# Kernel optimization log

Hardware: AMD Instinct MI355X
Metric: run time of the kernel (lower is better)

The kernel has to match this reference:

```python
import jax, jax.numpy as jnp
import numpy as np

SCALE_WEIGHT = 0.5 ** 0.5
B, C, T, S = 8, 512, 2048, 2048


def setup_inputs() -> dict:
    key = jax.random.key(0)
    ks = jax.random.split(key, 6)
    return {
        "base_target_emb": jax.random.normal(ks[0], (B, C, T, 1), dtype=jnp.float32),
        "input_from_dec": jax.random.normal(ks[1], (B, C, T, 1), dtype=jnp.float32),
        "encoder_out_top": jax.random.normal(ks[2], (B, C, S), dtype=jnp.float32),
        "encoder_out_combine": jax.random.normal(ks[3], (B, C, S), dtype=jnp.float32),
        "W": jax.random.normal(ks[4], (C, C), dtype=jnp.float32) * (1.0 / np.sqrt(C)),
        "b": jax.random.normal(ks[5], (C,), dtype=jnp.float32) * 0.01,
    }


def reference(base_target_emb, input_from_dec, encoder_out_top, encoder_out_combine, W, b):
    # seq_linear: per-token Linear over the channel dim. torch Linear: h = x @ W.T + b, W is [out,in]
    x = input_from_dec[..., 0]                                # [B,C,T]
    preatt = jnp.einsum('oc,bct->bot', W, x) + b[None, :, None]  # [B,C,T]
    target = (base_target_emb[..., 0] + preatt) * SCALE_WEIGHT   # [B,C,T]
    pre_attn = jnp.einsum('bct,bcs->bts', target, encoder_out_top)  # [B,T,S]
    attn = jax.nn.softmax(pre_attn, axis=2)                      # [B,T,S]
    ctx = jnp.einsum('bts,bcs->btc', attn, encoder_out_combine)  # [B,T,C]
    context_output = jnp.transpose(ctx, (0, 2, 1))[..., None]    # [B,C,T,1]
    return context_output, attn
```

## Files before the change

### kernel.cpp

```cpp
#include <hip/hip_runtime.h>
#include <cstddef>
#include <cstdint>

#define SCALE_WEIGHT 0.70710678118654752440f

static constexpr int B_ = 8, C_ = 512, T_ = 2048, S_ = 2048;
static constexpr size_t BCT_ = (size_t)B_ * C_ * T_;
static constexpr size_t BTS_ = (size_t)B_ * T_ * S_;

typedef _Float16 half_t;
typedef half_t half8  __attribute__((ext_vector_type(8)));
typedef half_t half4v __attribute__((ext_vector_type(4)));
typedef float  floatx4 __attribute__((ext_vector_type(4)));

__device__ __forceinline__ void gload_lds16(const void* g, void* l) {
    __builtin_amdgcn_global_load_lds(
        (const __attribute__((address_space(1))) void*)g,
        (__attribute__((address_space(3))) void*)l, 16, 0, 0);
}

__global__ __launch_bounds__(256) void transpose2_cvt_kernel(
    const float* __restrict__ x, const float* __restrict__ top,
    half_t* __restrict__ xT, half_t* __restrict__ topT)
{
    __shared__ float tile[64][65];
    const int z = blockIdx.z;
    const float* in = (z < 8) ? x : top;
    half_t* outp = (z < 8) ? xT : topT;
    const int b  = z & 7;
    const int r0 = blockIdx.y * 64, c0 = blockIdx.x * 64;
    const float* ib = in + (size_t)b * C_ * T_;
    half_t* ob = outp + (size_t)b * C_ * T_;
    const int t  = threadIdx.x;
    const int rr = t >> 4, cq = t & 15;
    #pragma unroll
    for (int i = 0; i < 4; ++i) {
        const int r = rr + i * 16;
        float4 v = *(const float4*)&ib[(size_t)(r0 + r) * T_ + c0 + cq * 4];
        tile[cq * 4 + 0][r] = v.x;
        tile[cq * 4 + 1][r] = v.y;
        tile[cq * 4 + 2][r] = v.z;
        tile[cq * 4 + 3][r] = v.w;
    }
    __syncthreads();
    const int cw = t >> 4, rq = (t & 15) * 4;
    #pragma unroll
    for (int i = 0; i < 4; ++i) {
        const int c = cw + i * 16;
        half4v h = {(half_t)tile[c][rq + 0], (half_t)tile[c][rq + 1],
                    (half_t)tile[c][rq + 2], (half_t)tile[c][rq + 3]};
        *(half4v*)&ob[(size_t)(c0 + c) * C_ + r0 + rq] = h;
    }
}

__global__ __launch_bounds__(256) void cvt2_f32_f16_kernel(
    const float* __restrict__ comb, half_t* __restrict__ combh,
    const float* __restrict__ W, half_t* __restrict__ Wh,
    int n4a, int n4tot)
{
    const int stride = gridDim.x * blockDim.x;
    for (int i = blockIdx.x * blockDim.x + threadIdx.x; i < n4tot; i += stride) {
        const float4* src; half4v* dst; int j;
        if (i < n4a) { src = (const float4*)comb; dst = (half4v*)combh; j = i; }
        else         { src = (const float4*)W;    dst = (half4v*)Wh;    j = i - n4a; }
        float4 v = src[j];
        dst[j] = (half4v){(half_t)v.x, (half_t)v.y, (half_t)v.z, (half_t)v.w};
    }
}

template<int EPI>
__global__ __launch_bounds__(256) void gemm_f16_db_kernel(
    const half_t* __restrict__ A, const half_t* __restrict__ Bm,
    float* __restrict__ Cout, half_t* __restrict__ CoutH,
    const float* __restrict__ base, const float* __restrict__ bias,
    int M, int N, int K, size_t sA, size_t sB, size_t sC)
{
    __shared__ __align__(128) half_t As[2][128 * 64];
    __shared__ __align__(128) half_t Bs[2][128 * 64];

    const int tid  = threadIdx.x;
    const int lane = tid & 63, w = tid >> 6;
    const int wr = w >> 1, wc = w & 1;
    const int b  = blockIdx.z;
    const int m0 = blockIdx.y * 128, n0 = blockIdx.x * 128;

    const half_t* Ab = A  + (size_t)b * sA;
    const half_t* Bb = Bm + (size_t)b * sB;

    const int lr = lane >> 3;
    const int sw = (lane & 7) ^ lr;
    const half_t* aG[4]; const half_t* bG[4];
    int dOff[4];
    #pragma unroll
    for (int i = 0; i < 4; ++i) {
        const int r = w * 32 + i * 8 + lr;
        aG[i] = Ab + (size_t)(m0 + r) * K + sw * 8;
        bG[i] = Bb + (size_t)(n0 + r) * K + sw * 8;
        dOff[i] = (w * 32 + i * 8) * 128;
    }

    const int fr = lane & 15, kg = lane >> 4;
    int aoff[4], boff[4];
    #pragma unroll
    for (int mi = 0; mi < 4; ++mi) {
        const int m = wr * 64 + mi * 16 + fr;
        aoff[mi] = m * 128 + ((kg ^ (m & 7)) << 4);
    }
    #pragma unroll
    for (int nj = 0; nj < 4; ++nj) {
        const int n = wc * 64 + nj * 16 + fr;
        boff[nj] = n * 128 + ((kg ^ (n & 7)) << 4);
    }

    floatx4 acc[4][4];
    #pragma unroll
    for (int mi = 0; mi < 4; ++mi)
        #pragma unroll
        for (int nj = 0; nj < 4; ++nj)
            acc[mi][nj] = (floatx4){0.f, 0.f, 0.f, 0.f};

    auto STAGE = [&](int t, int pg) {
        const int k0 = t * 64;
        char* Ad = (char*)As[pg];
        char* Bd = (char*)Bs[pg];
        #pragma unroll
        for (int i = 0; i < 4; ++i) {
            gload_lds16(aG[i] + k0, Ad + dOff[i]);
            gload_lds16(bG[i] + k0, Bd + dOff[i]);
        }
    };

    auto COMPUTE = [&](int pg) {
        const char* Ar = (const char*)As[pg];
        const char* Br = (const char*)Bs[pg];
        #pragma unroll
        for (int kk = 0; kk < 2; ++kk) {
            half8 af[4], bf[4];
            #pragma unroll
            for (int mi = 0; mi < 4; ++mi)
                af[mi] = *(const half8*)(Ar + (aoff[mi] ^ (kk << 6)));
            #pragma unroll
            for (int nj = 0; nj < 4; ++nj)
                bf[nj] = *(const half8*)(Br + (boff[nj] ^ (kk << 6)));
            #pragma unroll
            for (int mi = 0; mi < 4; ++mi)
                #pragma unroll
                for (int nj = 0; nj < 4; ++nj)
                    acc[mi][nj] = __builtin_amdgcn_mfma_f32_16x16x32_f16(
                        af[mi], bf[nj], acc[mi][nj], 0, 0, 0);
        }
    };

    const int NT = K >> 6;
    STAGE(0, 0);
    int cur = 0;
    for (int t = 0; t < NT - 1; ++t) {
        STAGE(t + 1, cur ^ 1);
        asm volatile("s_waitcnt vmcnt(8)" ::: "memory");
        __builtin_amdgcn_s_barrier();
        __builtin_amdgcn_sched_barrier(0);
        COMPUTE(cur);
        asm volatile("s_waitcnt lgkmcnt(0)" ::: "memory");
        __builtin_amdgcn_sched_barrier(0);
        __builtin_amdgcn_s_barrier();
        __builtin_amdgcn_sched_barrier(0);
        cur ^= 1;
    }
    asm volatile("s_waitcnt vmcnt(0)" ::: "memory");
    __builtin_amdgcn_s_barrier();
    __builtin_amdgcn_sched_barrier(0);
    COMPUTE(cur);

    if constexpr (EPI == 0) {
        float* Cb = Cout + (size_t)b * sC;
        #pragma unroll
        for (int mi = 0; mi < 4; ++mi) {
            const int row = m0 + wr * 64 + mi * 16 + (lane >> 4) * 4;
            #pragma unroll
            for (int nj = 0; nj < 4; ++nj) {
                const int col = n0 + wc * 64 + nj * 16 + (lane & 15);
                #pragma unroll
                for (int r = 0; r < 4; ++r)
                    Cb[(size_t)(row + r) * N + col] = acc[mi][nj][r];
            }
        }
    } else {
        half_t* Cb = CoutH + (size_t)b * sC;
        #pragma unroll
        for (int nj = 0; nj < 4; ++nj) {
            const int col = n0 + wc * 64 + nj * 16 + (lane & 15);
            const float bn = bias[col];
            const float* bp = base + ((size_t)b * N + col) * (size_t)M;
            #pragma unroll
            for (int mi = 0; mi < 4; ++mi) {
                const int row = m0 + wr * 64 + mi * 16 + (lane >> 4) * 4;
                #pragma unroll
                for (int r = 0; r < 4; ++r) {
                    float v = (acc[mi][nj][r] + bn + bp[row + r]) * SCALE_WEIGHT;
                    Cb[(size_t)(row + r) * N + col] = (half_t)v;
                }
            }
        }
    }
}

__global__ __launch_bounds__(256) void k2p_kernel(
    const half_t* __restrict__ A, const half_t* __restrict__ Bm,
    half_t* __restrict__ P, float* __restrict__ mArr, float* __restrict__ sArr)
{
    __shared__ __align__(128) half_t As[2][128 * 64];
    __shared__ __align__(128) half_t Bs[2][128 * 64];
    __shared__ float rmax[2][128];
    __shared__ float rsum[2][128];

    const int tid  = threadIdx.x;
    const int lane = tid & 63, w = tid >> 6;
    const int wr = w >> 1, wc = w & 1;
    const int b  = blockIdx.z;
    const int m0 = blockIdx.y * 128, n0 = blockIdx.x * 128;
    constexpr int K = C_;

    const half_t* Ab = A  + (size_t)b * T_ * C_;
    const half_t* Bb = Bm + (size_t)b * S_ * C_;

    const int lr = lane >> 3;
    const int sw = (lane & 7) ^ lr;
    const half_t* aG[4]; const half_t* bG[4];
    int dOff[4];
    #pragma unroll
    for (int i = 0; i < 4; ++i) {
        const int r = w * 32 + i * 8 + lr;
        aG[i] = Ab + (size_t)(m0 + r) * K + sw * 8;
        bG[i] = Bb + (size_t)(n0 + r) * K + sw * 8;
        dOff[i] = (w * 32 + i * 8) * 128;
    }

    const int fr = lane & 15, kg = lane >> 4;
    const int q4 = kg * 4;
    int aoff[4], boff[4];
    #pragma unroll
    for (int mi = 0; mi < 4; ++mi) {
        const int m = wr * 64 + mi * 16 + fr;
        aoff[mi] = m * 128 + ((kg ^ (m & 7)) << 4);
    }
    #pragma unroll
    for (int nj = 0; nj < 4; ++nj) {
        const int n = wc * 64 + nj * 16 + fr;
        boff[nj] = n * 128 + ((kg ^ (n & 7)) << 4);
    }

    floatx4 acc[4][4];
    #pragma unroll
    for (int mi = 0; mi < 4; ++mi)
        #pragma unroll
        for (int nj = 0; nj < 4; ++nj)
            acc[mi][nj] = (floatx4){0.f, 0.f, 0.f, 0.f};

    auto STAGE = [&](int t, int pg) {
        const int k0 = t * 64;
        char* Ad = (char*)As[pg];
        char* Bd = (char*)Bs[pg];
        #pragma unroll
        for (int i = 0; i < 4; ++i) {
            gload_lds16(aG[i] + k0, Ad + dOff[i]);
            gload_lds16(bG[i] + k0, Bd + dOff[i]);
        }
    };

    auto COMPUTE = [&](int pg) {
        const char* Ar = (const char*)As[pg];
        const char* Br = (const char*)Bs[pg];
        #pragma unroll
        for (int kk = 0; kk < 2; ++kk) {
            half8 af[4], bf[4];
            #pragma unroll
            for (int mi = 0; mi < 4; ++mi)
                af[mi] = *(const half8*)(Ar + (aoff[mi] ^ (kk << 6)));
            #pragma unroll
            for (int nj = 0; nj < 4; ++nj)
                bf[nj] = *(const half8*)(Br + (boff[nj] ^ (kk << 6)));
            #pragma unroll
            for (int mi = 0; mi < 4; ++mi)
                #pragma unroll
                for (int nj = 0; nj < 4; ++nj)
                    acc[mi][nj] = __builtin_amdgcn_mfma_f32_16x16x32_f16(
                        af[mi], bf[nj], acc[mi][nj], 0, 0, 0);
        }
    };

    constexpr int NT = K >> 6;
    STAGE(0, 0);
    int cur = 0;
    for (int t = 0; t < NT - 1; ++t) {
        STAGE(t + 1, cur ^ 1);
        asm volatile("s_waitcnt vmcnt(8)" ::: "memory");
        __builtin_amdgcn_s_barrier();
        __builtin_amdgcn_sched_barrier(0);
        COMPUTE(cur);
        asm volatile("s_waitcnt lgkmcnt(0)" ::: "memory");
        __builtin_amdgcn_sched_barrier(0);
        __builtin_amdgcn_s_barrier();
        __builtin_amdgcn_sched_barrier(0);
        cur ^= 1;
    }
    asm volatile("s_waitcnt vmcnt(0)" ::: "memory");
    __builtin_amdgcn_s_barrier();
    __builtin_amdgcn_sched_barrier(0);
    COMPUTE(cur);

    #pragma unroll
    for (int mi = 0; mi < 4; ++mi) {
        #pragma unroll
        for (int r = 0; r < 4; ++r) {
            float v = fmaxf(fmaxf(acc[mi][0][r], acc[mi][1][r]),
                            fmaxf(acc[mi][2][r], acc[mi][3][r]));
            v = fmaxf(v, __shfl_xor(v, 1));
            v = fmaxf(v, __shfl_xor(v, 2));
            v = fmaxf(v, __shfl_xor(v, 4));
            v = fmaxf(v, __shfl_xor(v, 8));
            if (fr == 0) rmax[wc][wr * 64 + mi * 16 + q4 + r] = v;
        }
    }
    __syncthreads();

    half_t* Pb = P + ((size_t)(b * T_ + m0)) * S_;
    #pragma unroll
    for (int mi = 0; mi < 4; ++mi) {
        #pragma unroll
        for (int r = 0; r < 4; ++r) {
            const int row = wr * 64 + mi * 16 + q4 + r;
            const float mC = fmaxf(rmax[0][row], rmax[1][row]);
            float s = 0.f;
            #pragma unroll
            for (int nj = 0; nj < 4; ++nj) {
                float pv = __expf(acc[mi][nj][r] - mC);
                s += pv;
                Pb[(size_t)row * S_ + n0 + wc * 64 + nj * 16 + fr] = (half_t)pv;
            }
            s += __shfl_xor(s, 1);
            s += __shfl_xor(s, 2);
            s += __shfl_xor(s, 4);
            s += __shfl_xor(s, 8);
            if (fr == 0) rsum[wc][row] = s;
        }
    }
    __syncthreads();

    if (tid < 128) {
        const float m = fmaxf(rmax[0][tid], rmax[1][tid]);
        const float s = rsum[0][tid] + rsum[1][tid];
        const size_t si = ((size_t)(b * 16 + (n0 >> 7))) * T_ + m0 + tid;
        mArr[si] = m;
        sArr[si] = s;
    }
}

__global__ __launch_bounds__(256) void k3b_kernel(
    const half_t* __restrict__ P, const float* __restrict__ mArr,
    const float* __restrict__ sArr, float* __restrict__ attnf,
    half_t* __restrict__ attnh)
{
    const int bid = blockIdx.x;
    const int b = bid >> 11, t = bid & 2047;
    const int tid = threadIdx.x;

    float mfin = -3.0e38f;
    #pragma unroll
    for (int j = 0; j < 16; ++j)
        mfin = fmaxf(mfin, mArr[((size_t)(b * 16 + j)) * T_ + t]);
    float sig = 0.f;
    #pragma unroll
    for (int j = 0; j < 16; ++j)
        sig += sArr[((size_t)(b * 16 + j)) * T_ + t] *
               __expf(mArr[((size_t)(b * 16 + j)) * T_ + t] - mfin);
    const float inv = 1.f / sig;
    const float f = __expf(mArr[((size_t)(b * 16 + (tid >> 4))) * T_ + t] - mfin) * inv;

    const size_t rb = (size_t)bid * S_ + tid * 8;
    half8 v = *(const half8*)&P[rb];
    float a0 = (float)v[0] * f, a1 = (float)v[1] * f;
    float a2 = (float)v[2] * f, a3 = (float)v[3] * f;
    float a4 = (float)v[4] * f, a5 = (float)v[5] * f;
    float a6 = (float)v[6] * f, a7 = (float)v[7] * f;
    *(float4*)&attnf[rb]     = (float4){a0, a1, a2, a3};
    *(float4*)&attnf[rb + 4] = (float4){a4, a5, a6, a7};
    half8 h;
    h[0] = (half_t)a0; h[1] = (half_t)a1; h[2] = (half_t)a2; h[3] = (half_t)a3;
    h[4] = (half_t)a4; h[5] = (half_t)a5; h[6] = (half_t)a6; h[7] = (half_t)a7;
    *(half8*)&attnh[rb] = h;
}

extern "C" void kernel_launch(void* const* d_in, const int* in_sizes, int n_in,
                              void* d_out, int out_size, void* d_ws, size_t ws_size,
                              hipStream_t stream) {
    const float* base = (const float*)d_in[0];
    const float* x    = (const float*)d_in[1];
    const float* top  = (const float*)d_in[2];
    const float* comb = (const float*)d_in[3];
    const float* W    = (const float*)d_in[4];
    const float* bias = (const float*)d_in[5];

    float* out   = (float*)d_out;
    float* ctx   = out;
    float* attnf = out + BCT_;

    half_t* xT   = (half_t*)d_out;
    half_t* topT = xT + BCT_;

    half_t* pws   = (half_t*)d_ws;
    half_t* attnh = pws + BTS_;
    half_t* combh = attnh + BTS_;
    half_t* Wh    = combh + (size_t)B_ * C_ * S_;
    half_t* tgtT  = Wh + (size_t)C_ * C_;
    float*  mArr  = (float*)(tgtT + BCT_);
    float*  sArr  = mArr + (size_t)B_ * 16 * T_;

    transpose2_cvt_kernel<<<dim3(T_ / 64, C_ / 64, 16), 256, 0, stream>>>(x, top, xT, topT);
    {
        const int n4a = (int)((size_t)B_ * C_ * S_ / 4);
        const int n4tot = n4a + C_ * C_ / 4;
        cvt2_f32_f16_kernel<<<2048, 256, 0, stream>>>(comb, combh, W, Wh, n4a, n4tot);
    }

    gemm_f16_db_kernel<1><<<dim3(C_ / 128, T_ / 128, B_), 256, 0, stream>>>(
        xT, Wh, nullptr, tgtT, base, bias,
        T_, C_, C_, (size_t)T_ * C_, 0, (size_t)T_ * C_);

    k2p_kernel<<<dim3(S_ / 128, T_ / 128, B_), 256, 0, stream>>>(
        tgtT, topT, pws, mArr, sArr);

    k3b_kernel<<<dim3(B_ * T_), 256, 0, stream>>>(pws, mArr, sArr, attnf, attnh);

    gemm_f16_db_kernel<0><<<dim3(T_ / 128, C_ / 128, B_), 256, 0, stream>>>(
        combh, attnh, ctx, nullptr, nullptr, nullptr,
        C_, T_, S_, (size_t)C_ * S_, (size_t)T_ * S_, (size_t)C_ * T_);
}
```

Measured before the change: 261.3 us.

## Unify GEMMs with K=32 stages, fold softmax scaling into final GEMM, drop attnh

Replaces the three separate GEMM kernels with one templated kernel that stages K in 32-wide steps, which halves LDS per block and may allow more blocks per CU. The batch index is taken from the low bits of a flat grid index. The softmax normalisation factors are now computed once in a small kernel. The final GEMM applies them on the fly to the unnormalised P tile in LDS, so the fp16 attention copy no longer needs to be written and read. The score GEMM writes P through LDS for coalesced stores. In exchange, P is scaled in fp16 inside the inner loop and each K step is shorter, which means more barriers.

```diff
diff --git a/kernel.cpp b/kernel.cpp
--- a/kernel.cpp
+++ b/kernel.cpp
@@ -68,48 +68,53 @@
     }
 }
 
-template<int EPI>
-__global__ __launch_bounds__(256) void gemm_f16_db_kernel(
+template<int MM, int NN, int KK, int EPI>
+__global__ __launch_bounds__(256) void gemm32_kernel(
     const half_t* __restrict__ A, const half_t* __restrict__ Bm,
-    float* __restrict__ Cout, half_t* __restrict__ CoutH,
+    size_t sA, size_t sB,
+    float* __restrict__ outF, half_t* __restrict__ outH,
     const float* __restrict__ base, const float* __restrict__ bias,
-    int M, int N, int K, size_t sA, size_t sB, size_t sC)
-{
-    __shared__ __align__(128) half_t As[2][128 * 64];
-    __shared__ __align__(128) half_t Bs[2][128 * 64];
-
-    const int tid  = threadIdx.x;
-    const int lane = tid & 63, w = tid >> 6;
+    float* __restrict__ mArr, float* __restrict__ sArr,
+    const float* __restrict__ fArr)
+{
+    constexpr int LDSSZ = (EPI == 1) ? 34816 : ((EPI == 2) ? 40960 : 32768);
+    __shared__ __align__(128) char smem[LDSSZ];
+
+    const int tid = threadIdx.x, lane = tid & 63, w = tid >> 6;
     const int wr = w >> 1, wc = w & 1;
-    const int b  = blockIdx.z;
-    const int m0 = blockIdx.y * 128, n0 = blockIdx.x * 128;
+
+    const int wgid = blockIdx.x;
+    const int b = wgid & 7;
+    const int tile = wgid >> 3;
+    constexpr int NXT = NN / 128;
+    constexpr int NMT = MM / 128;
+    int m0, n0;
+    if constexpr (EPI == 2) { n0 = (tile / NMT) * 128; m0 = (tile % NMT) * 128; }
+    else                    { n0 = (tile % NXT) * 128; m0 = (tile / NXT) * 128; }
 
     const half_t* Ab = A  + (size_t)b * sA;
     const half_t* Bb = Bm + (size_t)b * sB;
 
-    const int lr = lane >> 3;
-    const int sw = (lane & 7) ^ lr;
-    const half_t* aG[4]; const half_t* bG[4];
-    int dOff[4];
-    #pragma unroll
-    for (int i = 0; i < 4; ++i) {
-        const int r = w * 32 + i * 8 + lr;
-        aG[i] = Ab + (size_t)(m0 + r) * K + sw * 8;
-        bG[i] = Bb + (size_t)(n0 + r) * K + sw * 8;
-        dOff[i] = (w * 32 + i * 8) * 128;
-    }
+    const int lr = lane >> 2, sl = lane & 3;
+    const int ks = sl ^ (lr & 3);
+    const half_t* aG0 = Ab + (size_t)(m0 + w * 32      + lr) * KK + ks * 8;
+    const half_t* aG1 = Ab + (size_t)(m0 + w * 32 + 16 + lr) * KK + ks * 8;
+    const half_t* bG0 = Bb + (size_t)(n0 + w * 32      + lr) * KK + ks * 8;
+    const half_t* bG1 = Bb + (size_t)(n0 + w * 32 + 16 + lr) * KK + ks * 8;
+    const int dOff0 = (w * 32) * 64, dOff1 = (w * 32 + 16) * 64;
 
     const int fr = lane & 15, kg = lane >> 4;
+    const int q4 = kg * 4;
     int aoff[4], boff[4];
     #pragma unroll
     for (int mi = 0; mi < 4; ++mi) {
         const int m = wr * 64 + mi * 16 + fr;
-        aoff[mi] = m * 128 + ((kg ^ (m & 7)) << 4);
+        aoff[mi] = m * 64 + ((kg ^ (m & 3)) << 4);
     }
     #pragma unroll
     for (int nj = 0; nj < 4; ++nj) {
         const int n = wc * 64 + nj * 16 + fr;
-        boff[nj] = n * 128 + ((kg ^ (n & 7)) << 4);
+        boff[nj] = n * 64 + ((kg ^ (n & 3)) << 4);
     }
 
     floatx4 acc[4][4];
@@ -120,46 +125,59 @@
             acc[mi][nj] = (floatx4){0.f, 0.f, 0.f, 0.f};
 
     auto STAGE = [&](int t, int pg) {
-        const int k0 = t * 64;
-        char* Ad = (char*)As[pg];
-        char* Bd = (char*)Bs[pg];
-        #pragma unroll
-        for (int i = 0; i < 4; ++i) {
-            gload_lds16(aG[i] + k0, Ad + dOff[i]);
-            gload_lds16(bG[i] + k0, Bd + dOff[i]);
-        }
+        const int k0 = t * 32;
+        char* Ad = smem + pg * 8192;
+        char* Bd = smem + 16384 + pg * 8192;
+        gload_lds16(aG0 + k0, Ad + dOff0);
+        gload_lds16(aG1 + k0, Ad + dOff1);
+        gload_lds16(bG0 + k0, Bd + dOff0);
+        gload_lds16(bG1 + k0, Bd + dOff1);
     };
 
-    auto COMPUTE = [&](int pg) {
-        const char* Ar = (const char*)As[pg];
-        const char* Br = (const char*)Bs[pg];
-        #pragma unroll
-        for (int kk = 0; kk < 2; ++kk) {
-            half8 af[4], bf[4];
-            #pragma unroll
-            for (int mi = 0; mi < 4; ++mi)
-                af[mi] = *(const half8*)(Ar + (aoff[mi] ^ (kk << 6)));
+    auto COMPUTE = [&](int pg, int t) {
+        const char* Ar = smem + pg * 8192;
+        const char* Br = smem + 16384 + pg * 8192;
+        half8 af[4], bf[4];
+        #pragma unroll
+        for (int mi = 0; mi < 4; ++mi) af[mi] = *(const half8*)(Ar + aoff[mi]);
+        #pragma unroll
+        for (int nj = 0; nj < 4; ++nj) bf[nj] = *(const half8*)(Br + boff[nj]);
+        if constexpr (EPI == 2) {
+            const float* fls = (const float*)(smem + 32768);
+            const int st = t >> 2;
+            #pragma unroll
+            for (int nj = 0; nj < 4; ++nj) {
+                const half_t fh = (half_t)fls[st * 128 + wc * 64 + nj * 16 + fr];
+                #pragma unroll
+                for (int e = 0; e < 8; ++e) bf[nj][e] *= fh;
+            }
+        }
+        #pragma unroll
+        for (int mi = 0; mi < 4; ++mi)
             #pragma unroll
             for (int nj = 0; nj < 4; ++nj)
-                bf[nj] = *(const half8*)(Br + (boff[nj] ^ (kk << 6)));
-            #pragma unroll
-            for (int mi = 0; mi < 4; ++mi)
-                #pragma unroll
-                for (int nj = 0; nj < 4; ++nj)
-                    acc[mi][nj] = __builtin_amdgcn_mfma_f32_16x16x32_f16(
-                        af[mi], bf[nj], acc[mi][nj], 0, 0, 0);
-        }
+                acc[mi][nj] = __builtin_amdgcn_mfma_f32_16x16x32_f16(
+                    af[mi], bf[nj], acc[mi][nj], 0, 0, 0);
     };
 
-    const int NT = K >> 6;
+    if constexpr (EPI == 2) {
+        const float* fB = fArr + (size_t)b * 16 * T_;
+        #pragma unroll
+        for (int c = 0; c < 8; ++c)
+            gload_lds16(fB + (size_t)(2 * c + (lane >> 5)) * T_ + n0 + (lane & 31) * 4,
+                        smem + 32768 + c * 1024);
+    }
+    constexpr int NT = KK / 32;
     STAGE(0, 0);
     int cur = 0;
+    #pragma unroll 1
     for (int t = 0; t < NT - 1; ++t) {
         STAGE(t + 1, cur ^ 1);
-        asm volatile("s_waitcnt vmcnt(8)" ::: "memory");
+        __builtin_amdgcn_sched_barrier(0);
+        asm volatile("s_waitcnt vmcnt(4)" ::: "memory");
         __builtin_amdgcn_s_barrier();
         __builtin_amdgcn_sched_barrier(0);
-        COMPUTE(cur);
+        COMPUTE(cur, t);
         asm volatile("s_waitcnt lgkmcnt(0)" ::: "memory");
         __builtin_amdgcn_sched_barrier(0);
         __builtin_amdgcn_s_barrier();
@@ -169,225 +187,137 @@
     asm volatile("s_waitcnt vmcnt(0)" ::: "memory");
     __builtin_amdgcn_s_barrier();
     __builtin_amdgcn_sched_barrier(0);
-    COMPUTE(cur);
+    COMPUTE(cur, NT - 1);
 
     if constexpr (EPI == 0) {
-        float* Cb = Cout + (size_t)b * sC;
-        #pragma unroll
-        for (int mi = 0; mi < 4; ++mi) {
-            const int row = m0 + wr * 64 + mi * 16 + (lane >> 4) * 4;
-            #pragma unroll
-            for (int nj = 0; nj < 4; ++nj) {
-                const int col = n0 + wc * 64 + nj * 16 + (lane & 15);
-                #pragma unroll
-                for (int r = 0; r < 4; ++r)
-                    Cb[(size_t)(row + r) * N + col] = acc[mi][nj][r];
-            }
-        }
-    } else {
-        half_t* Cb = CoutH + (size_t)b * sC;
+        half_t* Cb = outH + (size_t)b * ((size_t)MM * NN);
         #pragma unroll
         for (int nj = 0; nj < 4; ++nj) {
-            const int col = n0 + wc * 64 + nj * 16 + (lane & 15);
+            const int col = n0 + wc * 64 + nj * 16 + fr;
             const float bn = bias[col];
-            const float* bp = base + ((size_t)b * N + col) * (size_t)M;
+            const float* bp = base + ((size_t)b * NN + col) * (size_t)MM;
             #pragma unroll
             for (int mi = 0; mi < 4; ++mi) {
-                const int row = m0 + wr * 64 + mi * 16 + (lane >> 4) * 4;
+                const int row = m0 + wr * 64 + mi * 16 + q4;
                 #pragma unroll
                 for (int r = 0; r < 4; ++r) {
                     float v = (acc[mi][nj][r] + bn + bp[row + r]) * SCALE_WEIGHT;
-                    Cb[(size_t)(row + r) * N + col] = (half_t)v;
+                    Cb[(size_t)(row + r) * NN + col] = (half_t)v;
                 }
             }
         }
-    }
-}
-
-__global__ __launch_bounds__(256) void k2p_kernel(
-    const half_t* __restrict__ A, const half_t* __restrict__ Bm,
-    half_t* __restrict__ P, float* __restrict__ mArr, float* __restrict__ sArr)
-{
-    __shared__ __align__(128) half_t As[2][128 * 64];
-    __shared__ __align__(128) half_t Bs[2][128 * 64];
-    __shared__ float rmax[2][128];
-    __shared__ float rsum[2][128];
-
-    const int tid  = threadIdx.x;
-    const int lane = tid & 63, w = tid >> 6;
-    const int wr = w >> 1, wc = w & 1;
-    const int b  = blockIdx.z;
-    const int m0 = blockIdx.y * 128, n0 = blockIdx.x * 128;
-    constexpr int K = C_;
-
-    const half_t* Ab = A  + (size_t)b * T_ * C_;
-    const half_t* Bb = Bm + (size_t)b * S_ * C_;
-
-    const int lr = lane >> 3;
-    const int sw = (lane & 7) ^ lr;
-    const half_t* aG[4]; const half_t* bG[4];
-    int dOff[4];
-    #pragma unroll
-    for (int i = 0; i < 4; ++i) {
-        const int r = w * 32 + i * 8 + lr;
-        aG[i] = Ab + (size_t)(m0 + r) * K + sw * 8;
-        bG[i] = Bb + (size_t)(n0 + r) * K + sw * 8;
-        dOff[i] = (w * 32 + i * 8) * 128;
-    }
-
-    const int fr = lane & 15, kg = lane >> 4;
-    const int q4 = kg * 4;
-    int aoff[4], boff[4];
-    #pragma unroll
-    for (int mi = 0; mi < 4; ++mi) {
-        const int m = wr * 64 + mi * 16 + fr;
-        aoff[mi] = m * 128 + ((kg ^ (m & 7)) << 4);
-    }
-    #pragma unroll
-    for (int nj = 0; nj < 4; ++nj) {
-        const int n = wc * 64 + nj * 16 + fr;
-        boff[nj] = n * 128 + ((kg ^ (n & 7)) << 4);
-    }
-
-    floatx4 acc[4][4];
-    #pragma unroll
-    for (int mi = 0; mi < 4; ++mi)
-        #pragma unroll
-        for (int nj = 0; nj < 4; ++nj)
-            acc[mi][nj] = (floatx4){0.f, 0.f, 0.f, 0.f};
-
-    auto STAGE = [&](int t, int pg) {
-        const int k0 = t * 64;
-        char* Ad = (char*)As[pg];
-        char* Bd = (char*)Bs[pg];
-        #pragma unroll
-        for (int i = 0; i < 4; ++i) {
-            gload_lds16(aG[i] + k0, Ad + dOff[i]);
-            gload_lds16(bG[i] + k0, Bd + dOff[i]);
-        }
-    };
-
-    auto COMPUTE = [&](int pg) {
-        const char* Ar = (const char*)As[pg];
-        const char* Br = (const char*)Bs[pg];
-        #pragma unroll
-        for (int kk = 0; kk < 2; ++kk) {
-            half8 af[4], bf[4];
-            #pragma unroll
-            for (int mi = 0; mi < 4; ++mi)
-                af[mi] = *(const half8*)(Ar + (aoff[mi] ^ (kk << 6)));
-            #pragma unroll
-            for (int nj = 0; nj < 4; ++nj)
-                bf[nj] = *(const half8*)(Br + (boff[nj] ^ (kk << 6)));
-            #pragma unroll
-            for (int mi = 0; mi < 4; ++mi)
+    } else if constexpr (EPI == 2) {
+        float* Cb = outF + (size_t)b * ((size_t)MM * NN);
+        #pragma unroll
+        for (int mi = 0; mi < 4; ++mi) {
+            const int row = m0 + wr * 64 + mi * 16 + q4;
+            #pragma unroll
+            for (int nj = 0; nj < 4; ++nj) {
+                const int col = n0 + wc * 64 + nj * 16 + fr;
                 #pragma unroll
-                for (int nj = 0; nj < 4; ++nj)
-                    acc[mi][nj] = __builtin_amdgcn_mfma_f32_16x16x32_f16(
-                        af[mi], bf[nj], acc[mi][nj], 0, 0, 0);
-        }
-    };
-
-    constexpr int NT = K >> 6;
-    STAGE(0, 0);
-    int cur = 0;
-    for (int t = 0; t < NT - 1; ++t) {
-        STAGE(t + 1, cur ^ 1);
-        asm volatile("s_waitcnt vmcnt(8)" ::: "memory");
-        __builtin_amdgcn_s_barrier();
-        __builtin_amdgcn_sched_barrier(0);
-        COMPUTE(cur);
-        asm volatile("s_waitcnt lgkmcnt(0)" ::: "memory");
-        __builtin_amdgcn_sched_barrier(0);
-        __builtin_amdgcn_s_barrier();
-        __builtin_amdgcn_sched_barrier(0);
-        cur ^= 1;
-    }
-    asm volatile("s_waitcnt vmcnt(0)" ::: "memory");
-    __builtin_amdgcn_s_barrier();
-    __builtin_amdgcn_sched_barrier(0);
-    COMPUTE(cur);
-
-    #pragma unroll
-    for (int mi = 0; mi < 4; ++mi) {
-        #pragma unroll
-        for (int r = 0; r < 4; ++r) {
-            float v = fmaxf(fmaxf(acc[mi][0][r], acc[mi][1][r]),
-                            fmaxf(acc[mi][2][r], acc[mi][3][r]));
-            v = fmaxf(v, __shfl_xor(v, 1));
-            v = fmaxf(v, __shfl_xor(v, 2));
-            v = fmaxf(v, __shfl_xor(v, 4));
-            v = fmaxf(v, __shfl_xor(v, 8));
-            if (fr == 0) rmax[wc][wr * 64 + mi * 16 + q4 + r] = v;
-        }
-    }
-    __syncthreads();
-
-    half_t* Pb = P + ((size_t)(b * T_ + m0)) * S_;
-    #pragma unroll
-    for (int mi = 0; mi < 4; ++mi) {
-        #pragma unroll
-        for (int r = 0; r < 4; ++r) {
-            const int row = wr * 64 + mi * 16 + q4 + r;
-            const float mC = fmaxf(rmax[0][row], rmax[1][row]);
-            float s = 0.f;
-            #pragma unroll
-            for (int nj = 0; nj < 4; ++nj) {
-                float pv = __expf(acc[mi][nj][r] - mC);
-                s += pv;
-                Pb[(size_t)row * S_ + n0 + wc * 64 + nj * 16 + fr] = (half_t)pv;
-            }
-            s += __shfl_xor(s, 1);
-            s += __shfl_xor(s, 2);
-            s += __shfl_xor(s, 4);
-            s += __shfl_xor(s, 8);
-            if (fr == 0) rsum[wc][row] = s;
-        }
-    }
-    __syncthreads();
-
-    if (tid < 128) {
-        const float m = fmaxf(rmax[0][tid], rmax[1][tid]);
-        const float s = rsum[0][tid] + rsum[1][tid];
-        const size_t si = ((size_t)(b * 16 + (n0 >> 7))) * T_ + m0 + tid;
-        mArr[si] = m;
-        sArr[si] = s;
-    }
-}
-
-__global__ __launch_bounds__(256) void k3b_kernel(
-    const half_t* __restrict__ P, const float* __restrict__ mArr,
-    const float* __restrict__ sArr, float* __restrict__ attnf,
-    half_t* __restrict__ attnh)
+                for (int r = 0; r < 4; ++r)
+                    Cb[(size_t)(row + r) * NN + col] = acc[mi][nj][r];
+            }
+        }
+    } else {
+        __syncthreads();
+        float* rmax = (float*)(smem + 32768);
+        float* rsum = (float*)(smem + 32768 + 1024);
+
+        #pragma unroll
+        for (int mi = 0; mi < 4; ++mi)
+            #pragma unroll
+            for (int r = 0; r < 4; ++r) {
+                float v = fmaxf(fmaxf(acc[mi][0][r], acc[mi][1][r]),
+                                fmaxf(acc[mi][2][r], acc[mi][3][r]));
+                v = fmaxf(v, __shfl_xor(v, 1));
+                v = fmaxf(v, __shfl_xor(v, 2));
+                v = fmaxf(v, __shfl_xor(v, 4));
+                v = fmaxf(v, __shfl_xor(v, 8));
+                if (fr == 0) rmax[wc * 128 + wr * 64 + mi * 16 + q4 + r] = v;
+            }
+        __syncthreads();
+
+        #pragma unroll
+        for (int mi = 0; mi < 4; ++mi)
+            #pragma unroll
+            for (int r = 0; r < 4; ++r) {
+                const int row = wr * 64 + mi * 16 + q4 + r;
+                const float mC = fmaxf(rmax[row], rmax[128 + row]);
+                float s = 0.f;
+                #pragma unroll
+                for (int nj = 0; nj < 4; ++nj) {
+                    const int col = wc * 64 + nj * 16 + fr;
+                    float pv = __expf(acc[mi][nj][r] - mC);
+                    s += pv;
+                    *(half_t*)(smem + row * 256 + ((col * 2) ^ ((row & 7) << 4))) =
+                        (half_t)pv;
+                }
+                s += __shfl_xor(s, 1);
+                s += __shfl_xor(s, 2);
+                s += __shfl_xor(s, 4);
+                s += __shfl_xor(s, 8);
+                if (fr == 0) rsum[wc * 128 + row] = s;
+            }
+        __syncthreads();
+
+        if (tid < 128) {
+            const float m = fmaxf(rmax[tid], rmax[128 + tid]);
+            const float s = rsum[tid] + rsum[128 + tid];
+            const size_t si = ((size_t)(b * 16 + (n0 >> 7))) * (size_t)MM + m0 + tid;
+            mArr[si] = m;
+            sArr[si] = s;
+        }
+
+        half_t* Pb = outH + ((size_t)b * MM + m0) * (size_t)NN + n0;
+        const int rlo = tid >> 4, slot = tid & 15;
+        #pragma unroll
+        for (int pp = 0; pp < 8; ++pp) {
+            const int row = pp * 16 + rlo;
+            const int lb = row * 256 + ((slot * 16) ^ ((row & 7) << 4));
+            half8 v = *(const half8*)(smem + lb);
+            *(half8*)&Pb[(size_t)row * NN + slot * 8] = v;
+        }
+    }
+}
+
+__global__ __launch_bounds__(256) void kf_kernel(
+    const float* __restrict__ mArr, const float* __restrict__ sArr,
+    float* __restrict__ fArr)
+{
+    const int gid = blockIdx.x * 256 + threadIdx.x;
+    const int b = gid >> 11, t = gid & 2047;
+    float mv[16];
+    float mfin = -3.0e38f;
+    #pragma unroll
+    for (int j = 0; j < 16; ++j) {
+        mv[j] = mArr[((size_t)(b * 16 + j)) * T_ + t];
+        mfin = fmaxf(mfin, mv[j]);
+    }
+    float sig = 0.f;
+    #pragma unroll
+    for (int j = 0; j < 16; ++j)
+        sig += sArr[((size_t)(b * 16 + j)) * T_ + t] * __expf(mv[j] - mfin);
+    const float inv = 1.f / sig;
+    #pragma unroll
+    for (int j = 0; j < 16; ++j)
+        fArr[((size_t)(b * 16 + j)) * T_ + t] = __expf(mv[j] - mfin) * inv;
+}
+
+__global__ __launch_bounds__(256) void k3n_kernel(
+    const half_t* __restrict__ P, const float* __restrict__ fArr,
+    float* __restrict__ attnf)
 {
     const int bid = blockIdx.x;
     const int b = bid >> 11, t = bid & 2047;
     const int tid = threadIdx.x;
-
-    float mfin = -3.0e38f;
-    #pragma unroll
-    for (int j = 0; j < 16; ++j)
-        mfin = fmaxf(mfin, mArr[((size_t)(b * 16 + j)) * T_ + t]);
-    float sig = 0.f;
-    #pragma unroll
-    for (int j = 0; j < 16; ++j)
-        sig += sArr[((size_t)(b * 16 + j)) * T_ + t] *
-               __expf(mArr[((size_t)(b * 16 + j)) * T_ + t] - mfin);
-    const float inv = 1.f / sig;
-    const float f = __expf(mArr[((size_t)(b * 16 + (tid >> 4))) * T_ + t] - mfin) * inv;
-
+    const float f = fArr[((size_t)(b * 16 + (tid >> 4))) * T_ + t];
     const size_t rb = (size_t)bid * S_ + tid * 8;
     half8 v = *(const half8*)&P[rb];
-    float a0 = (float)v[0] * f, a1 = (float)v[1] * f;
-    float a2 = (float)v[2] * f, a3 = (float)v[3] * f;
-    float a4 = (float)v[4] * f, a5 = (float)v[5] * f;
-    float a6 = (float)v[6] * f, a7 = (float)v[7] * f;
-    *(float4*)&attnf[rb]     = (float4){a0, a1, a2, a3};
-    *(float4*)&attnf[rb + 4] = (float4){a4, a5, a6, a7};
-    half8 h;
-    h[0] = (half_t)a0; h[1] = (half_t)a1; h[2] = (half_t)a2; h[3] = (half_t)a3;
-    h[4] = (half_t)a4; h[5] = (half_t)a5; h[6] = (half_t)a6; h[7] = (half_t)a7;
-    *(half8*)&attnh[rb] = h;
+    float4 o0 = {(float)v[0] * f, (float)v[1] * f, (float)v[2] * f, (float)v[3] * f};
+    float4 o1 = {(float)v[4] * f, (float)v[5] * f, (float)v[6] * f, (float)v[7] * f};
+    *(float4*)&attnf[rb]     = o0;
+    *(float4*)&attnf[rb + 4] = o1;
 }
 
 extern "C" void kernel_launch(void* const* d_in, const int* in_sizes, int n_in,
@@ -408,12 +338,12 @@
     half_t* topT = xT + BCT_;
 
     half_t* pws   = (half_t*)d_ws;
-    half_t* attnh = pws + BTS_;
-    half_t* combh = attnh + BTS_;
+    half_t* combh = pws + BTS_;
     half_t* Wh    = combh + (size_t)B_ * C_ * S_;
     half_t* tgtT  = Wh + (size_t)C_ * C_;
     float*  mArr  = (float*)(tgtT + BCT_);
     float*  sArr  = mArr + (size_t)B_ * 16 * T_;
+    float*  fArr  = sArr + (size_t)B_ * 16 * T_;
 
     transpose2_cvt_kernel<<<dim3(T_ / 64, C_ / 64, 16), 256, 0, stream>>>(x, top, xT, topT);
     {
@@ -422,16 +352,19 @@
         cvt2_f32_f16_kernel<<<2048, 256, 0, stream>>>(comb, combh, W, Wh, n4a, n4tot);
     }
 
-    gemm_f16_db_kernel<1><<<dim3(C_ / 128, T_ / 128, B_), 256, 0, stream>>>(
-        xT, Wh, nullptr, tgtT, base, bias,
-        T_, C_, C_, (size_t)T_ * C_, 0, (size_t)T_ * C_);
-
-    k2p_kernel<<<dim3(S_ / 128, T_ / 128, B_), 256, 0, stream>>>(
-        tgtT, topT, pws, mArr, sArr);
-
-    k3b_kernel<<<dim3(B_ * T_), 256, 0, stream>>>(pws, mArr, sArr, attnf, attnh);
-
-    gemm_f16_db_kernel<0><<<dim3(T_ / 128, C_ / 128, B_), 256, 0, stream>>>(
-        combh, attnh, ctx, nullptr, nullptr, nullptr,
-        C_, T_, S_, (size_t)C_ * S_, (size_t)T_ * S_, (size_t)C_ * T_);
-}
+    gemm32_kernel<2048, 512, 512, 0><<<512, 256, 0, stream>>>(
+        xT, Wh, (size_t)T_ * C_, 0,
+        nullptr, tgtT, base, bias, nullptr, nullptr, nullptr);
+
+    gemm32_kernel<2048, 2048, 512, 1><<<2048, 256, 0, stream>>>(
+        tgtT, topT, (size_t)T_ * C_, (size_t)S_ * C_,
+        nullptr, pws, nullptr, nullptr, mArr, sArr, nullptr);
+
+    kf_kernel<<<64, 256, 0, stream>>>(mArr, sArr, fArr);
+
+    k3n_kernel<<<B_ * T_, 256, 0, stream>>>(pws, fArr, attnf);
+
+    gemm32_kernel<512, 2048, 2048, 2><<<512, 256, 0, stream>>>(
+        combh, pws, (size_t)C_ * S_, (size_t)T_ * S_,
+        ctx, nullptr, nullptr, nullptr, nullptr, nullptr, fArr);
+}
```

Result: faster. 235.2 us (-10.0%).
